# Performance work log

Measured on AMD Instinct MI355X. Metric: run time of the kernel, lower is better.

Reference implementation:

```python
import jax, jax.numpy as jnp
import numpy as np

B, S, H, D = 4, 2048, 16, 64


def setup_inputs() -> dict:
    key = jax.random.key(0)
    kq, kk, kv, kl = jax.random.split(key, 4)
    qs = jax.random.normal(kq, (B, S, H, D), dtype=jnp.float32)
    ks = jax.random.normal(kk, (B, S, H, D), dtype=jnp.float32)
    vs = jax.random.normal(kv, (B, S, H, D), dtype=jnp.float32)
    # valid lengths in [S//2, S] so no sequence is fully masked out
    valid_lens = jax.random.randint(kl, (B,), S // 2, S + 1, dtype=jnp.int32)
    return {"qs": qs, "ks": ks, "vs": vs, "valid_lens": valid_lens}


def reference(qs, ks, vs, valid_lens):
    # ScanAttention == exact softmax attention (FlashAttention-2 is an
    # IO-aware reformulation of the same math). qs scaled by 1/sqrt(D).
    d = qs.shape[-1]
    scale = 1.0 / jnp.sqrt(jnp.asarray(d, qs.dtype))
    # scores: [B, H, Q, K]
    scores = jnp.einsum('bqhd,bkhd->bhqk', qs * scale, ks)
    # key mask from valid_lens: position k is valid iff k < valid_lens[b]
    k_len = ks.shape[1]
    ks_mask = jnp.arange(k_len)[None, :] < valid_lens[:, None]  # [B, K]
    scores = jnp.where(ks_mask[:, None, None, :], scores, -jnp.inf)
    attn = jax.nn.softmax(scores, axis=-1)
    ctx = jnp.einsum('bhqk,bkhd->bqhd', attn, vs)
    return ctx
```

## Files before the change

### kernel.cpp

```cpp
#include <hip/hip_runtime.h>
#include <hip/hip_bf16.h>

typedef __bf16 bf16x8 __attribute__((ext_vector_type(8)));
typedef float  f32x4  __attribute__((ext_vector_type(4)));
typedef float  f32x16 __attribute__((ext_vector_type(16)));
typedef float  f4     __attribute__((ext_vector_type(4)));
typedef unsigned int u32;
typedef u32 u32x4 __attribute__((ext_vector_type(4)));

#define MFMA16(a,b,c) __builtin_amdgcn_mfma_f32_16x16x32_bf16(a,b,c,0,0,0)
#define MFMA32(a,b,c) __builtin_amdgcn_mfma_f32_32x32x16_bf16(a,b,c,0,0,0)

constexpr int   Bc = 4, Sc = 2048, Hc = 16, Dc = 64;
constexpr int   HD  = Hc * Dc;
constexpr int   SHD = Sc * HD;
constexpr float SCALE = 0.125f;
constexpr float LOG2E = 1.4426950408889634f;
constexpr float QSC   = SCALE * LOG2E;
constexpr float NEG   = -1e30f;
constexpr int   HEAD_ELEMS = Sc * Dc;
constexpr size_t KV_ELEMS  = (size_t)Bc * Hc * HEAD_ELEMS;

__global__ __launch_bounds__(256) void prep2(
    const float* __restrict__ K, const float* __restrict__ V,
    __bf16* __restrict__ Kf, __bf16* __restrict__ Vf)
{
    __shared__ __align__(16) __bf16 KT[64][80];
    __shared__ __align__(16) __bf16 VT[64][80];

    const int bid = blockIdx.x;
    const int st  = bid & 31;
    const int h   = (bid >> 5) & 15;
    const int b   = bid >> 9;
    const int tid = threadIdx.x;
    const int sl  = tid >> 2;
    const int d0  = (tid & 3) * 16;
    const size_t iof = ((size_t)(b * 2048 + st * 64 + sl) * 16 + h) * 64 + d0;

    #pragma unroll
    for (int q = 0; q < 2; ++q) {
        f4 a = __builtin_nontemporal_load((const f4*)(K + iof + q * 8));
        f4 c = __builtin_nontemporal_load((const f4*)(K + iof + q * 8 + 4));
        bf16x8 w;
        w[0]=(__bf16)a.x; w[1]=(__bf16)a.y; w[2]=(__bf16)a.z; w[3]=(__bf16)a.w;
        w[4]=(__bf16)c.x; w[5]=(__bf16)c.y; w[6]=(__bf16)c.z; w[7]=(__bf16)c.w;
        *(bf16x8*)&KT[sl][d0 + q * 8] = w;
    }
    #pragma unroll
    for (int q = 0; q < 2; ++q) {
        f4 a = __builtin_nontemporal_load((const f4*)(V + iof + q * 8));
        f4 c = __builtin_nontemporal_load((const f4*)(V + iof + q * 8 + 4));
        bf16x8 w;
        w[0]=(__bf16)a.x; w[1]=(__bf16)a.y; w[2]=(__bf16)a.z; w[3]=(__bf16)a.w;
        w[4]=(__bf16)c.x; w[5]=(__bf16)c.y; w[6]=(__bf16)c.z; w[7]=(__bf16)c.w;
        *(bf16x8*)&VT[sl][d0 + q * 8] = w;
    }
    __syncthreads();

    const size_t hbase = (size_t)(b * 16 + h) * HEAD_ELEMS;

    #pragma unroll
    for (int it = 0; it < 2; ++it) {
        const int idx = it * 256 + tid;
        const int tl  = idx >> 8;
        const int dk  = (idx >> 6) & 3;
        const int ln  = idx & 63;
        const int l31 = ln & 31, lhi = ln >> 5;
        bf16x8 w = *(const bf16x8*)&KT[tl * 32 + l31][dk * 16 + lhi * 8];
        *(bf16x8*)(Kf + hbase + (size_t)(((st * 2 + tl) * 4 + dk) * 512 + ln * 8)) = w;
    }
    #pragma unroll
    for (int it = 0; it < 2; ++it) {
        const int idx  = it * 256 + tid;
        const int tl   = idx >> 8;
        const int dblk = (idx >> 7) & 1;
        const int kt2  = (idx >> 6) & 1;
        const int ln   = idx & 63;
        const int l31  = ln & 31, lhi = ln >> 5;
        bf16x8 w;
        #pragma unroll
        for (int j = 0; j < 8; ++j)
            w[j] = VT[tl * 32 + kt2 * 16 + lhi * 8 + j][dblk * 32 + l31];
        *(bf16x8*)(Vf + hbase +
            (size_t)(((((st * 2 + tl) * 2 + dblk) * 2 + kt2)) * 512 + ln * 8)) = w;
    }
}

__global__ __launch_bounds__(256, 3) void fattn6(
    const float* __restrict__ Q, const __bf16* __restrict__ Kf,
    const __bf16* __restrict__ Vf, const int* __restrict__ VL,
    float* __restrict__ O)
{
    __shared__ float Lacc[2][64][65];
    __shared__ float Lsum[2][64];

    const int bid  = blockIdx.x;
    const int xcd  = bid & 7;
    const int hbit = (bid >> 3) & 1;
    const int p    = (bid >> 4) & 15;
    const int z    = bid >> 8;
    const int h    = xcd + 8 * hbit;
    const int b    = (z + p) & 3;
    const int w    = threadIdx.x >> 6;
    const int sub  = w & 1;
    const int half = w >> 1;
    const int head = b * 16 + h;
    const int lane = threadIdx.x & 63;
    const int l31  = lane & 31;
    const int hi   = lane >> 5;
    const int vl   = VL[b];

    const size_t qbase = (size_t)b * SHD + (size_t)h * Dc;
    const __bf16* kfh = Kf + (size_t)head * HEAD_ELEMS + lane * 8;
    const __bf16* vfh = Vf + (size_t)head * HEAD_ELEMS + lane * 8;
    const int qrow0 = (p * 2 + sub) * 64;

    bf16x8 qfA[4], qfB[4];
    #pragma unroll
    for (int qt2 = 0; qt2 < 2; ++qt2) {
        const float* qp = Q + qbase + (size_t)(qrow0 + qt2 * 32 + l31) * HD + hi * 8;
        #pragma unroll
        for (int dk = 0; dk < 4; ++dk) {
            f4 x0 = __builtin_nontemporal_load((const f4*)(qp + dk * 16));
            f4 x1 = __builtin_nontemporal_load((const f4*)(qp + dk * 16 + 4));
            bf16x8 f;
            f[0]=(__bf16)(x0.x*QSC); f[1]=(__bf16)(x0.y*QSC);
            f[2]=(__bf16)(x0.z*QSC); f[3]=(__bf16)(x0.w*QSC);
            f[4]=(__bf16)(x1.x*QSC); f[5]=(__bf16)(x1.y*QSC);
            f[6]=(__bf16)(x1.z*QSC); f[7]=(__bf16)(x1.w*QSC);
            if (qt2 == 0) qfA[dk] = f; else qfB[dk] = f;
        }
    }

    f32x16 aA0, aA1, aB0, aB1;
    #pragma unroll
    for (int i = 0; i < 16; ++i) { aA0[i]=0.f; aA1[i]=0.f; aB0[i]=0.f; aB1[i]=0.f; }
    float lsumA = 0.f, lsumB = 0.f;

    const int ntot = (vl + 31) >> 5;
    const int nh0  = (ntot + 1) >> 1;
    const int t0   = half ? nh0 : 0;
    const int t1   = half ? ntot : nh0;
    const bool hastail = (vl & 31) != 0;

    for (int t = t0; t < t1; ++t) {
        const size_t off = (size_t)t * 2048;

        bf16x8 kf0 = *(const bf16x8*)(kfh + off);
        bf16x8 kf1 = *(const bf16x8*)(kfh + off + 512);
        bf16x8 kf2 = *(const bf16x8*)(kfh + off + 1024);
        bf16x8 kf3 = *(const bf16x8*)(kfh + off + 1536);

        f32x16 sA, sB;
        #pragma unroll
        for (int i = 0; i < 16; ++i) { sA[i] = 0.f; sB[i] = 0.f; }
        sA = MFMA32(kf0, qfA[0], sA);  sB = MFMA32(kf0, qfB[0], sB);
        sA = MFMA32(kf1, qfA[1], sA);  sB = MFMA32(kf1, qfB[1], sB);
        sA = MFMA32(kf2, qfA[2], sA);  sB = MFMA32(kf2, qfB[2], sB);
        sA = MFMA32(kf3, qfA[3], sA);  sB = MFMA32(kf3, qfB[3], sB);

        bf16x8 vf0 = *(const bf16x8*)(vfh + off);
        bf16x8 vf1 = *(const bf16x8*)(vfh + off + 512);
        bf16x8 vf2 = *(const bf16x8*)(vfh + off + 1024);
        bf16x8 vf3 = *(const bf16x8*)(vfh + off + 1536);

        if (t == ntot - 1 && hastail) {
            const int kv0 = t * 32;
            #pragma unroll
            for (int i = 0; i < 16; ++i) {
                const int key = kv0 + (i & 3) + 8 * (i >> 2) + 4 * hi;
                if (key >= vl) { sA[i] = NEG; sB[i] = NEG; }
            }
        }

        #pragma unroll
        for (int i = 0; i < 16; ++i) {
            sA[i] = __builtin_amdgcn_exp2f(sA[i]);
            sB[i] = __builtin_amdgcn_exp2f(sB[i]);
        }
        {
            float uA = ((sA[0]+sA[1])+(sA[2]+sA[3])) + ((sA[4]+sA[5])+(sA[6]+sA[7]));
            float vA = ((sA[8]+sA[9])+(sA[10]+sA[11])) + ((sA[12]+sA[13])+(sA[14]+sA[15]));
            lsumA += uA + vA;
            float uB = ((sB[0]+sB[1])+(sB[2]+sB[3])) + ((sB[4]+sB[5])+(sB[6]+sB[7]));
            float vB = ((sB[8]+sB[9])+(sB[10]+sB[11])) + ((sB[12]+sB[13])+(sB[14]+sB[15]));
            lsumB += uB + vB;
        }

        bf16x8 apA[2], apB[2];
        #pragma unroll
        for (int kt = 0; kt < 2; ++kt) {
            u32 a0, a1, a2, a3, b0, b1, b2, b3;
            asm("v_cvt_pk_bf16_f32 %0, %1, %2" : "=v"(a0) : "v"(sA[8*kt+0]), "v"(sA[8*kt+1]));
            asm("v_cvt_pk_bf16_f32 %0, %1, %2" : "=v"(a1) : "v"(sA[8*kt+2]), "v"(sA[8*kt+3]));
            asm("v_cvt_pk_bf16_f32 %0, %1, %2" : "=v"(a2) : "v"(sA[8*kt+4]), "v"(sA[8*kt+5]));
            asm("v_cvt_pk_bf16_f32 %0, %1, %2" : "=v"(a3) : "v"(sA[8*kt+6]), "v"(sA[8*kt+7]));
            asm("v_permlane32_swap_b32 %0, %1" : "+v"(a0), "+v"(a2));
            asm("v_permlane32_swap_b32 %0, %1" : "+v"(a1), "+v"(a3));
            u32x4 fwA; fwA.x = a0; fwA.y = a1; fwA.z = a2; fwA.w = a3;
            apA[kt] = __builtin_bit_cast(bf16x8, fwA);
            asm("v_cvt_pk_bf16_f32 %0, %1, %2" : "=v"(b0) : "v"(sB[8*kt+0]), "v"(sB[8*kt+1]));
            asm("v_cvt_pk_bf16_f32 %0, %1, %2" : "=v"(b1) : "v"(sB[8*kt+2]), "v"(sB[8*kt+3]));
            asm("v_cvt_pk_bf16_f32 %0, %1, %2" : "=v"(b2) : "v"(sB[8*kt+4]), "v"(sB[8*kt+5]));
            asm("v_cvt_pk_bf16_f32 %0, %1, %2" : "=v"(b3) : "v"(sB[8*kt+6]), "v"(sB[8*kt+7]));
            asm("v_permlane32_swap_b32 %0, %1" : "+v"(b0), "+v"(b2));
            asm("v_permlane32_swap_b32 %0, %1" : "+v"(b1), "+v"(b3));
            u32x4 fwB; fwB.x = b0; fwB.y = b1; fwB.z = b2; fwB.w = b3;
            apB[kt] = __builtin_bit_cast(bf16x8, fwB);
        }

        aA0 = MFMA32(vf0, apA[0], aA0);  aB0 = MFMA32(vf0, apB[0], aB0);
        aA0 = MFMA32(vf1, apA[1], aA0);  aB0 = MFMA32(vf1, apB[1], aB0);
        aA1 = MFMA32(vf2, apA[0], aA1);  aB1 = MFMA32(vf2, apB[0], aB1);
        aA1 = MFMA32(vf3, apA[1], aA1);  aB1 = MFMA32(vf3, apB[1], aB1);
    }

    const float lA = lsumA + __shfl_xor(lsumA, 32);
    const float lB = lsumB + __shfl_xor(lsumB, 32);

    if (half) {
        #pragma unroll
        for (int qd = 0; qd < 4; ++qd) {
            f4 v0, v1, v2, v3;
            v0.x=aA0[4*qd+0]; v0.y=aA0[4*qd+1]; v0.z=aA0[4*qd+2]; v0.w=aA0[4*qd+3];
            v1.x=aA1[4*qd+0]; v1.y=aA1[4*qd+1]; v1.z=aA1[4*qd+2]; v1.w=aA1[4*qd+3];
            v2.x=aB0[4*qd+0]; v2.y=aB0[4*qd+1]; v2.z=aB0[4*qd+2]; v2.w=aB0[4*qd+3];
            v3.x=aB1[4*qd+0]; v3.y=aB1[4*qd+1]; v3.z=aB1[4*qd+2]; v3.w=aB1[4*qd+3];
            *(f4*)&Lacc[sub][l31][qd*8 + 4*hi]           = v0;
            *(f4*)&Lacc[sub][l31][32 + qd*8 + 4*hi]      = v1;
            *(f4*)&Lacc[sub][32 + l31][qd*8 + 4*hi]      = v2;
            *(f4*)&Lacc[sub][32 + l31][32 + qd*8 + 4*hi] = v3;
        }
        Lsum[sub][l31]      = lA;
        Lsum[sub][32 + l31] = lB;
    }
    __syncthreads();
    if (!half) {
        const float linvA = 1.0f / (lA + Lsum[sub][l31]);
        const float linvB = 1.0f / (lB + Lsum[sub][32 + l31]);
        float* opA = O + qbase + (size_t)(qrow0 + l31) * HD;
        float* opB = O + qbase + (size_t)(qrow0 + 32 + l31) * HD;
        #pragma unroll
        for (int qd = 0; qd < 4; ++qd) {
            f4 p0 = *(const f4*)&Lacc[sub][l31][qd*8 + 4*hi];
            f4 p1 = *(const f4*)&Lacc[sub][l31][32 + qd*8 + 4*hi];
            f4 p2 = *(const f4*)&Lacc[sub][32 + l31][qd*8 + 4*hi];
            f4 p3 = *(const f4*)&Lacc[sub][32 + l31][32 + qd*8 + 4*hi];
            f4 o0, o1, o2, o3;
            o0.x=(aA0[4*qd+0]+p0.x)*linvA; o0.y=(aA0[4*qd+1]+p0.y)*linvA;
            o0.z=(aA0[4*qd+2]+p0.z)*linvA; o0.w=(aA0[4*qd+3]+p0.w)*linvA;
            o1.x=(aA1[4*qd+0]+p1.x)*linvA; o1.y=(aA1[4*qd+1]+p1.y)*linvA;
            o1.z=(aA1[4*qd+2]+p1.z)*linvA; o1.w=(aA1[4*qd+3]+p1.w)*linvA;
            o2.x=(aB0[4*qd+0]+p2.x)*linvB; o2.y=(aB0[4*qd+1]+p2.y)*linvB;
            o2.z=(aB0[4*qd+2]+p2.z)*linvB; o2.w=(aB0[4*qd+3]+p2.w)*linvB;
            o3.x=(aB1[4*qd+0]+p3.x)*linvB; o3.y=(aB1[4*qd+1]+p3.y)*linvB;
            o3.z=(aB1[4*qd+2]+p3.z)*linvB; o3.w=(aB1[4*qd+3]+p3.w)*linvB;
            *(f4*)(opA + qd * 8 + 4 * hi)      = o0;
            *(f4*)(opA + 32 + qd * 8 + 4 * hi) = o1;
            *(f4*)(opB + qd * 8 + 4 * hi)      = o2;
            *(f4*)(opB + 32 + qd * 8 + 4 * hi) = o3;
        }
    }
}

__global__ __launch_bounds__(256, 2) void fattn_fb(
    const float* __restrict__ Q, const float* __restrict__ K,
    const float* __restrict__ V, const int* __restrict__ VL,
    float* __restrict__ O)
{
    __shared__ __bf16 Vts[64 * 64];
    __shared__ __bf16 Pl[4][32 * 64];
    const int bid = blockIdx.x;
    const int qt = bid & 15, h = (bid >> 4) & 15, b = bid >> 8;
    const int tid = threadIdx.x, wid = tid >> 6, lane = tid & 63;
    const int li = lane & 15, lg = lane >> 4;
    const int vl = VL[b];
    const size_t base = (size_t)b * SHD + (size_t)h * Dc;
    bf16x8 aq[2][2];
    const int qrow0 = qt * 128 + wid * 32;
    #pragma unroll
    for (int m = 0; m < 2; ++m) {
        const float* qp = Q + base + (size_t)(qrow0 + m * 16 + li) * HD + lg * 8;
        #pragma unroll
        for (int ks = 0; ks < 2; ++ks) {
            float4 x0 = *(const float4*)(qp + ks * 32);
            float4 x1 = *(const float4*)(qp + ks * 32 + 4);
            bf16x8 f;
            f[0]=(__bf16)(x0.x*QSC); f[1]=(__bf16)(x0.y*QSC);
            f[2]=(__bf16)(x0.z*QSC); f[3]=(__bf16)(x0.w*QSC);
            f[4]=(__bf16)(x1.x*QSC); f[5]=(__bf16)(x1.y*QSC);
            f[6]=(__bf16)(x1.z*QSC); f[7]=(__bf16)(x1.w*QSC);
            aq[m][ks] = f;
        }
    }
    bf16x8 bones;
    #pragma unroll
    for (int j = 0; j < 8; ++j) bones[j] = (__bf16)1.0f;
    f32x4 acc[2][4]; float mst[2][4], lst[2][4];
    #pragma unroll
    for (int m = 0; m < 2; ++m) {
        #pragma unroll
        for (int r = 0; r < 4; ++r) { mst[m][r] = NEG; lst[m][r] = 0.f; }
        #pragma unroll
        for (int dt = 0; dt < 4; ++dt)
            #pragma unroll
            for (int r = 0; r < 4; ++r) acc[m][dt][r] = 0.f;
    }
    const int ntiles = (vl + 63) >> 6;
    const int sd = tid & 63, skb = (tid >> 6) * 8;
    const float* vpd = V + base + sd;
    for (int t = 0; t < ntiles; ++t) {
        const int kv0 = t * 64;
        __syncthreads();
        #pragma unroll
        for (int rep = 0; rep < 2; ++rep) {
            const int kb2 = skb + rep * 32;
            bf16x8 pk;
            #pragma unroll
            for (int j = 0; j < 8; ++j) pk[j] = (__bf16)vpd[(size_t)(kv0+kb2+j)*HD];
            *(bf16x8*)&Vts[(sd*64+kb2) ^ ((sd&7)<<3)] = pk;
        }
        __syncthreads();
        f32x4 s[2][4];
        #pragma unroll
        for (int m = 0; m < 2; ++m)
            #pragma unroll
            for (int nt2 = 0; nt2 < 4; ++nt2)
                #pragma unroll
                for (int r = 0; r < 4; ++r) s[m][nt2][r] = 0.f;
        #pragma unroll
        for (int nt2 = 0; nt2 < 4; ++nt2) {
            const float* kp = K + base + (size_t)(kv0+nt2*16+li)*HD + lg*8;
            #pragma unroll
            for (int ks = 0; ks < 2; ++ks) {
                float4 x0 = *(const float4*)(kp + ks*32);
                float4 x1 = *(const float4*)(kp + ks*32 + 4);
                bf16x8 f;
                f[0]=(__bf16)x0.x; f[1]=(__bf16)x0.y; f[2]=(__bf16)x0.z; f[3]=(__bf16)x0.w;
                f[4]=(__bf16)x1.x; f[5]=(__bf16)x1.y; f[6]=(__bf16)x1.z; f[7]=(__bf16)x1.w;
                #pragma unroll
                for (int m = 0; m < 2; ++m) s[m][nt2] = MFMA16(aq[m][ks], f, s[m][nt2]);
            }
        }
        bool kva[4];
        #pragma unroll
        for (int nt2 = 0; nt2 < 4; ++nt2) kva[nt2] = (kv0 + nt2*16 + li) < vl;
        #pragma unroll
        for (int m = 0; m < 2; ++m)
            #pragma unroll
            for (int nt2 = 0; nt2 < 4; ++nt2)
                #pragma unroll
                for (int r = 0; r < 4; ++r)
                    if (!kva[nt2]) s[m][nt2][r] = NEG;
        #pragma unroll
        for (int m = 0; m < 2; ++m) {
            #pragma unroll
            for (int r = 0; r < 4; ++r) {
                float tmx = fmaxf(fmaxf(s[m][0][r], s[m][1][r]),
                                  fmaxf(s[m][2][r], s[m][3][r]));
                tmx = fmaxf(tmx, __shfl_xor(tmx, 1));
                tmx = fmaxf(tmx, __shfl_xor(tmx, 2));
                tmx = fmaxf(tmx, __shfl_xor(tmx, 4));
                tmx = fmaxf(tmx, __shfl_xor(tmx, 8));
                const float mn = fmaxf(mst[m][r], tmx);
                const float fac = __builtin_amdgcn_exp2f(mst[m][r] - mn);
                mst[m][r] = mn; lst[m][r] *= fac;
                #pragma unroll
                for (int dt = 0; dt < 4; ++dt) acc[m][dt][r] *= fac;
                const int qr = m*16 + lg*4 + r, swz = (qr & 7) << 3;
                #pragma unroll
                for (int nt2 = 0; nt2 < 4; ++nt2)
                    Pl[wid][(qr*64 + nt2*16 + li) ^ swz] =
                        (__bf16)__builtin_amdgcn_exp2f(s[m][nt2][r] - mn);
            }
        }
        bf16x8 ap[2][2];
        #pragma unroll
        for (int m = 0; m < 2; ++m) {
            const int qr = m*16 + li, swz = (qr & 7) << 3;
            #pragma unroll
            for (int ks = 0; ks < 2; ++ks)
                ap[m][ks] = *(bf16x8*)&Pl[wid][(qr*64 + ks*32 + lg*8) ^ swz];
        }
        #pragma unroll
        for (int m = 0; m < 2; ++m) {
            f32x4 rs;
            #pragma unroll
            for (int r = 0; r < 4; ++r) rs[r] = 0.f;
            rs = MFMA16(ap[m][0], bones, rs);
            rs = MFMA16(ap[m][1], bones, rs);
            #pragma unroll
            for (int r = 0; r < 4; ++r) lst[m][r] += rs[r];
        }
        #pragma unroll
        for (int dt = 0; dt < 4; ++dt) {
            const int d = dt*16 + li, swz = (d & 7) << 3;
            #pragma unroll
            for (int ks = 0; ks < 2; ++ks) {
                bf16x8 bv = *(bf16x8*)&Vts[(d*64 + ks*32 + lg*8) ^ swz];
                #pragma unroll
                for (int m = 0; m < 2; ++m)
                    acc[m][dt] = MFMA16(ap[m][ks], bv, acc[m][dt]);
            }
        }
    }
    #pragma unroll
    for (int m = 0; m < 2; ++m) {
        #pragma unroll
        for (int r = 0; r < 4; ++r) {
            const float inv = 1.0f / lst[m][r];
            float* op = O + base + (size_t)(qrow0 + m*16 + lg*4 + r) * HD;
            #pragma unroll
            for (int dt = 0; dt < 4; ++dt) op[dt*16 + li] = acc[m][dt][r] * inv;
        }
    }
}

extern "C" void kernel_launch(void* const* d_in, const int* in_sizes, int n_in,
                              void* d_out, int out_size, void* d_ws, size_t ws_size,
                              hipStream_t stream) {
    (void)in_sizes; (void)n_in; (void)out_size;
    const float* q    = (const float*)d_in[0];
    const float* k    = (const float*)d_in[1];
    const float* v    = (const float*)d_in[2];
    const int*   vlen = (const int*)d_in[3];
    float*       out  = (float*)d_out;
    const size_t need = 2 * KV_ELEMS * sizeof(__bf16);
    if (ws_size >= need) {
        __bf16* kfp = (__bf16*)d_ws;
        __bf16* vfp = kfp + KV_ELEMS;
        prep2<<<dim3(2048), 256, 0, stream>>>(k, v, kfp, vfp);
        fattn6<<<dim3(1024), 256, 0, stream>>>(q, kfp, vfp, vlen, out);
    } else {
        fattn_fb<<<dim3(1024), 256, 0, stream>>>(q, k, v, vlen, out);
    }
}
```

Before: 109.9 us.

## Split each block's KV range across four waves sharing one query tile

Each block now handles one 64-row query tile instead of two, and all four waves split the key range into quarters rather than two waves per tile splitting it in halves. The grid doubles to 2048 blocks. Partial accumulators and row sums are combined in LDS with shared-memory atomic adds, and all 256 threads cooperatively normalize and write the output. This aims for more parallelism and better load balance across CUs, at the cost of reloading Q per block, more atomic LDS traffic and an extra barrier.

```diff
diff --git a/kernel.cpp b/kernel.cpp
--- a/kernel.cpp
+++ b/kernel.cpp
@@ -86,24 +86,24 @@
     }
 }
 
-__global__ __launch_bounds__(256, 3) void fattn6(
+__global__ __launch_bounds__(256, 3) void fattn7(
     const float* __restrict__ Q, const __bf16* __restrict__ Kf,
     const __bf16* __restrict__ Vf, const int* __restrict__ VL,
     float* __restrict__ O)
 {
-    __shared__ float Lacc[2][64][65];
-    __shared__ float Lsum[2][64];
+    __shared__ float Lacc[64][65];
+    __shared__ float Lsum[64];
 
     const int bid  = blockIdx.x;
     const int xcd  = bid & 7;
     const int hbit = (bid >> 3) & 1;
     const int p    = (bid >> 4) & 15;
-    const int z    = bid >> 8;
+    const int q4   = (bid >> 8) & 1;
+    const int z    = bid >> 9;
     const int h    = xcd + 8 * hbit;
     const int b    = (z + p) & 3;
-    const int w    = threadIdx.x >> 6;
-    const int sub  = w & 1;
-    const int half = w >> 1;
+    const int qg   = q4 * 16 + p;
+    const int quarter = threadIdx.x >> 6;
     const int head = b * 16 + h;
     const int lane = threadIdx.x & 63;
     const int l31  = lane & 31;
@@ -113,7 +113,7 @@
     const size_t qbase = (size_t)b * SHD + (size_t)h * Dc;
     const __bf16* kfh = Kf + (size_t)head * HEAD_ELEMS + lane * 8;
     const __bf16* vfh = Vf + (size_t)head * HEAD_ELEMS + lane * 8;
-    const int qrow0 = (p * 2 + sub) * 64;
+    const int qrow0 = qg * 64;
 
     bf16x8 qfA[4], qfB[4];
     #pragma unroll
@@ -138,9 +138,10 @@
     float lsumA = 0.f, lsumB = 0.f;
 
     const int ntot = (vl + 31) >> 5;
-    const int nh0  = (ntot + 1) >> 1;
-    const int t0   = half ? nh0 : 0;
-    const int t1   = half ? ntot : nh0;
+    const int base = ntot >> 2;
+    const int rem  = ntot & 3;
+    const int t0   = quarter * base + (quarter < rem ? quarter : rem);
+    const int t1   = t0 + base + (quarter < rem ? 1 : 0);
     const bool hastail = (vl & 31) != 0;
 
     for (int t = t0; t < t1; ++t) {
@@ -218,7 +219,7 @@
     const float lA = lsumA + __shfl_xor(lsumA, 32);
     const float lB = lsumB + __shfl_xor(lsumB, 32);
 
-    if (half) {
+    if (quarter == 0) {
         #pragma unroll
         for (int qd = 0; qd < 4; ++qd) {
             f4 v0, v1, v2, v3;
@@ -226,39 +227,41 @@
             v1.x=aA1[4*qd+0]; v1.y=aA1[4*qd+1]; v1.z=aA1[4*qd+2]; v1.w=aA1[4*qd+3];
             v2.x=aB0[4*qd+0]; v2.y=aB0[4*qd+1]; v2.z=aB0[4*qd+2]; v2.w=aB0[4*qd+3];
             v3.x=aB1[4*qd+0]; v3.y=aB1[4*qd+1]; v3.z=aB1[4*qd+2]; v3.w=aB1[4*qd+3];
-            *(f4*)&Lacc[sub][l31][qd*8 + 4*hi]           = v0;
-            *(f4*)&Lacc[sub][l31][32 + qd*8 + 4*hi]      = v1;
-            *(f4*)&Lacc[sub][32 + l31][qd*8 + 4*hi]      = v2;
-            *(f4*)&Lacc[sub][32 + l31][32 + qd*8 + 4*hi] = v3;
-        }
-        Lsum[sub][l31]      = lA;
-        Lsum[sub][32 + l31] = lB;
+            *(f4*)&Lacc[l31][qd*8 + 4*hi]           = v0;
+            *(f4*)&Lacc[l31][32 + qd*8 + 4*hi]      = v1;
+            *(f4*)&Lacc[32 + l31][qd*8 + 4*hi]      = v2;
+            *(f4*)&Lacc[32 + l31][32 + qd*8 + 4*hi] = v3;
+        }
+        if (hi == 0) { Lsum[l31] = lA; Lsum[32 + l31] = lB; }
     }
     __syncthreads();
-    if (!half) {
-        const float linvA = 1.0f / (lA + Lsum[sub][l31]);
-        const float linvB = 1.0f / (lB + Lsum[sub][32 + l31]);
-        float* opA = O + qbase + (size_t)(qrow0 + l31) * HD;
-        float* opB = O + qbase + (size_t)(qrow0 + 32 + l31) * HD;
+    if (quarter != 0) {
         #pragma unroll
         for (int qd = 0; qd < 4; ++qd) {
-            f4 p0 = *(const f4*)&Lacc[sub][l31][qd*8 + 4*hi];
-            f4 p1 = *(const f4*)&Lacc[sub][l31][32 + qd*8 + 4*hi];
-            f4 p2 = *(const f4*)&Lacc[sub][32 + l31][qd*8 + 4*hi];
-            f4 p3 = *(const f4*)&Lacc[sub][32 + l31][32 + qd*8 + 4*hi];
-            f4 o0, o1, o2, o3;
-            o0.x=(aA0[4*qd+0]+p0.x)*linvA; o0.y=(aA0[4*qd+1]+p0.y)*linvA;
-            o0.z=(aA0[4*qd+2]+p0.z)*linvA; o0.w=(aA0[4*qd+3]+p0.w)*linvA;
-            o1.x=(aA1[4*qd+0]+p1.x)*linvA; o1.y=(aA1[4*qd+1]+p1.y)*linvA;
-            o1.z=(aA1[4*qd+2]+p1.z)*linvA; o1.w=(aA1[4*qd+3]+p1.w)*linvA;
-            o2.x=(aB0[4*qd+0]+p2.x)*linvB; o2.y=(aB0[4*qd+1]+p2.y)*linvB;
-            o2.z=(aB0[4*qd+2]+p2.z)*linvB; o2.w=(aB0[4*qd+3]+p2.w)*linvB;
-            o3.x=(aB1[4*qd+0]+p3.x)*linvB; o3.y=(aB1[4*qd+1]+p3.y)*linvB;
-            o3.z=(aB1[4*qd+2]+p3.z)*linvB; o3.w=(aB1[4*qd+3]+p3.w)*linvB;
-            *(f4*)(opA + qd * 8 + 4 * hi)      = o0;
-            *(f4*)(opA + 32 + qd * 8 + 4 * hi) = o1;
-            *(f4*)(opB + qd * 8 + 4 * hi)      = o2;
-            *(f4*)(opB + 32 + qd * 8 + 4 * hi) = o3;
+            #pragma unroll
+            for (int rr = 0; rr < 4; ++rr) {
+                const int d = qd * 8 + 4 * hi + rr;
+                atomicAdd(&Lacc[l31][d],           aA0[4*qd+rr]);
+                atomicAdd(&Lacc[l31][32 + d],      aA1[4*qd+rr]);
+                atomicAdd(&Lacc[32 + l31][d],      aB0[4*qd+rr]);
+                atomicAdd(&Lacc[32 + l31][32 + d], aB1[4*qd+rr]);
+            }
+        }
+        if (hi == 0) { atomicAdd(&Lsum[l31], lA); atomicAdd(&Lsum[32 + l31], lB); }
+    }
+    __syncthreads();
+
+    {
+        const int tid = threadIdx.x;
+        const int qq  = tid >> 2;
+        const int dc  = (tid & 3) * 16;
+        const float linv = 1.0f / Lsum[qq];
+        float* op = O + qbase + (size_t)(qrow0 + qq) * HD + dc;
+        #pragma unroll
+        for (int j = 0; j < 4; ++j) {
+            f4 v = *(const f4*)&Lacc[qq][dc + j * 4];
+            v.x *= linv; v.y *= linv; v.z *= linv; v.w *= linv;
+            *(f4*)(op + j * 4) = v;
         }
     }
 }
@@ -430,7 +433,7 @@
         __bf16* kfp = (__bf16*)d_ws;
         __bf16* vfp = kfp + KV_ELEMS;
         prep2<<<dim3(2048), 256, 0, stream>>>(k, v, kfp, vfp);
-        fattn6<<<dim3(1024), 256, 0, stream>>>(q, kfp, vfp, vlen, out);
+        fattn7<<<dim3(2048), 256, 0, stream>>>(q, kfp, vfp, vlen, out);
     } else {
         fattn_fb<<<dim3(1024), 256, 0, stream>>>(q, k, v, vlen, out);
     }
```

After: 197.6 us. 1.8x slower.
